# Kernel optimization log

Measured on AMD Instinct MI355X. Metric: run time of the kernel, lower is better.

## Reference

```python
import jax, jax.numpy as jnp
import numpy as np

D_MODEL, D_STATE, D_CONV, D_INNER, DT_RANK, K = 96, 16, 3, 192, 6, 4
B, H, W = 1, 64, 64


def setup_inputs() -> dict:
    key = jax.random.key(0)
    ks = jax.random.split(key, 10)
    x = jax.random.normal(ks[0], (B, H, W, D_MODEL), jnp.float32)
    in_proj_w = jax.random.normal(ks[1], (2 * D_INNER, D_MODEL), jnp.float32) * 0.02
    conv_w = jax.random.normal(ks[2], (D_INNER, 1, D_CONV, D_CONV), jnp.float32) * 0.1
    conv_b = jnp.zeros((D_INNER,), jnp.float32)
    x_proj_w = jax.random.normal(ks[3], (K, DT_RANK + 2 * D_STATE, D_INNER), jnp.float32) * 0.02
    dt_std = DT_RANK ** -0.5
    dt_w = jax.random.uniform(ks[4], (K, D_INNER, DT_RANK), jnp.float32, -dt_std, dt_std)
    # dt bias init: inv-softplus of dt ~ logUniform(1e-3, 1e-1)
    u = jax.random.uniform(ks[5], (K, D_INNER), jnp.float32)
    dt = jnp.exp(u * (np.log(0.1) - np.log(0.001)) + np.log(0.001)).clip(1e-4)
    dt_b = dt + jnp.log(-jnp.expm1(-dt))
    A_logs = jnp.log(jnp.broadcast_to(jnp.arange(1, D_STATE + 1, dtype=jnp.float32), (K * D_INNER, D_STATE)))
    Ds = jnp.ones((K * D_INNER,), jnp.float32)
    ln_g = jnp.ones((D_INNER,), jnp.float32)
    ln_b = jnp.zeros((D_INNER,), jnp.float32)
    out_proj_w = jax.random.normal(ks[6], (D_MODEL, D_INNER), jnp.float32) * 0.02
    return dict(x=x, in_proj_w=in_proj_w, conv_w=conv_w, conv_b=conv_b, x_proj_w=x_proj_w,
                dt_w=dt_w, dt_b=dt_b, A_logs=A_logs, Ds=Ds, ln_g=ln_g, ln_b=ln_b,
                out_proj_w=out_proj_w)


def _ss2d(x, in_proj_w, conv_w, conv_b, x_proj_w, dt_w, dt_b, A_logs, Ds, ln_g, ln_b, out_proj_w):
    b, h, w, c = x.shape
    L = h * w
    d = conv_w.shape[0]            # d_inner
    n = A_logs.shape[1]            # d_state
    r = dt_w.shape[2]              # dt_rank
    # in_proj + split
    xz = jnp.einsum('bhwc,ec->bhwe', x, in_proj_w)
    xx, z = xz[..., :d], xz[..., d:]
    # depthwise conv (NCHW) + SiLU
    xc = xx.transpose(0, 3, 1, 2)
    pad = (D_CONV - 1) // 2
    xc = jax.lax.conv_general_dilated(xc, conv_w, (1, 1), [(pad, pad), (pad, pad)],
                                      feature_group_count=d) + conv_b[None, :, None, None]
    xc = jax.nn.silu(xc)
    # 4 scan directions: HW, WH, and their reverses
    x_hw = xc.reshape(b, d, L)
    x_wh = xc.transpose(0, 1, 3, 2).reshape(b, d, L)
    xs = jnp.stack([x_hw, x_wh, x_hw[..., ::-1], x_wh[..., ::-1]], axis=1)  # (b,K,d,L)
    x_dbl = jnp.einsum('bkdl,kcd->bkcl', xs, x_proj_w)
    dts, Bs, Cs = x_dbl[:, :, :r], x_dbl[:, :, r:r + n], x_dbl[:, :, r + n:]
    dts = jnp.einsum('bkrl,kdr->bkdl', dts, dt_w)
    delta = jax.nn.softplus(dts + dt_b[None, :, :, None])        # (b,K,d,L)
    A = -jnp.exp(A_logs).reshape(K, d, n)
    # time-major scanned inputs
    dA = jnp.exp(jnp.einsum('bkdl,kdn->lbkdn', delta, A))        # (L,b,K,d,n)
    dBu = jnp.einsum('bkdl,bknl,bkdl->lbkdn', delta, Bs, xs)
    Ct = Cs.transpose(3, 0, 1, 2)                                # (L,b,K,n)
    def step(hst, inp):
        dA_t, dBu_t, C_t = inp
        hst = dA_t * hst + dBu_t
        return hst, jnp.einsum('bkdn,bkn->bkd', hst, C_t)
    h0 = jnp.zeros((b, K, d, n), jnp.float32)
    _, ys = jax.lax.scan(step, h0, (dA, dBu, Ct))                # ys: (L,b,K,d)
    out_y = ys.transpose(1, 2, 3, 0) + xs * Ds.reshape(K, d)[None, :, :, None]
    # recombine directions
    inv = out_y[:, 2:4][..., ::-1]
    y1 = out_y[:, 0]
    y2 = inv[:, 0]
    wh = out_y[:, 1].reshape(b, d, w, h).transpose(0, 1, 3, 2).reshape(b, d, L)
    invwh = inv[:, 1].reshape(b, d, w, h).transpose(0, 1, 3, 2).reshape(b, d, L)
    y = (y1 + y2 + wh + invwh).transpose(0, 2, 1).reshape(b, h, w, d)
    # LayerNorm (eps=1e-5, torch default)
    mu = y.mean(-1, keepdims=True)
    var = ((y - mu) ** 2).mean(-1, keepdims=True)
    y = (y - mu) * jax.lax.rsqrt(var + 1e-5) * ln_g + ln_b
    y = y * jax.nn.silu(z)
    return jnp.einsum('bhwd,cd->bhwc', y, out_proj_w)


def reference(x, in_proj_w, conv_w, conv_b, x_proj_w, dt_w, dt_b, A_logs, Ds, ln_g, ln_b, out_proj_w):
    return _ss2d(x, in_proj_w, conv_w, conv_b, x_proj_w, dt_w, dt_b, A_logs, Ds, ln_g, ln_b, out_proj_w)
```

## Files before the change

kernel.cpp:

```cpp
#include <hip/hip_runtime.h>
#include <hip/hip_bf16.h>

#define LL 4096
#define DM 96
#define DI 192
#define NS 16
#define RK 6
#define RKP 8
#define KD 4
#define CPROJ 38
#define NCH (KD*DI)
#define NC (KD*DI*NS)
#define PT 32
#define WS 196
#define OT 8
#define L2E 1.44269504f

__device__ __forceinline__ float bf2f(unsigned short u){
  unsigned int x = ((unsigned int)u) << 16;
  return __uint_as_float(x);
}
__device__ __forceinline__ float b2f(__hip_bfloat16 v){ return __bfloat162float(v); }

__device__ __forceinline__ void detect_bf16(const unsigned short* __restrict__ xh, int tid, int* sflag){
  if (tid < 64){
    unsigned short u = xh[2*tid];
    int e = (u >> 7) & 0xFF;
    int sane = (e >= 107 && e <= 131) ? 1 : 0;
    unsigned long long m = __ballot(sane);
    if (tid == 0) *sflag = (__popcll(m) >= 32) ? 1 : 0;
  }
}

__device__ __forceinline__ int dir_map(int k, int t){
  if (k==0) return t;
  if (k==1) return ((t&63)<<6) | (t>>6);
  if (k==2) return 4095 - t;
  int u = 4095 - t; return ((u&63)<<6) | (u>>6);
}

struct P12 { const void* p[12]; };

__global__ void __launch_bounds__(384) k_inprojcvt(P12 ptrs, float* __restrict__ cvt,
                         float* __restrict__ xx, float* __restrict__ z) {
  __shared__ float xr[8*DM];
  __shared__ int sflag;
  int tid = threadIdx.x;
  detect_bf16((const unsigned short*)ptrs.p[0], tid, &sflag);
  __syncthreads();
  int f = sflag;
  if (blockIdx.x >= LL/8){
    const int off[12] = {0,36864,38592,38784,67968,72576,73344,85632,86400,86592,86784,105216};
    int i = (blockIdx.x - LL/8)*384 + tid + 36864;
    if (i < 105216){
      int j = 1;
      #pragma unroll
      for (int s = 2; s < 11; s++) if (i >= off[s]) j = s;
      int e = i - off[j];
      const void* src = ptrs.p[j+1];
      cvt[i] = f ? b2f(((const __hip_bfloat16*)src)[e]) : ((const float*)src)[e];
    }
    return;
  }
  int l0 = blockIdx.x * 8;
  if (f){
    const __hip_bfloat16* xb = (const __hip_bfloat16*)ptrs.p[0] + (size_t)l0*DM;
    for (int i = tid; i < 8*DM; i += 384) xr[i] = b2f(xb[i]);
  } else {
    const float* xf = (const float*)ptrs.p[0] + (size_t)l0*DM;
    for (int i = tid; i < 8*DM; i += 384) xr[i] = xf[i];
  }
  __syncthreads();
  int e = tid;
  float acc[8];
  #pragma unroll
  for (int i=0;i<8;i++) acc[i]=0.f;
  const float4* xr4 = (const float4*)xr;
  if (f){
    const ushort4* wb = (const ushort4*)((const unsigned short*)ptrs.p[1] + (size_t)e*DM);
    #pragma unroll 4
    for (int c4=0;c4<DM/4;c4++){
      ushort4 uv = wb[c4];
      float4 wv = make_float4(bf2f(uv.x), bf2f(uv.y), bf2f(uv.z), bf2f(uv.w));
      #pragma unroll
      for (int i=0;i<8;i++){
        float4 xv = xr4[i*24 + c4];
        acc[i] = fmaf(wv.x,xv.x,fmaf(wv.y,xv.y,fmaf(wv.z,xv.z,fmaf(wv.w,xv.w,acc[i]))));
      }
    }
  } else {
    const float4* wr4 = (const float4*)((const float*)ptrs.p[1] + (size_t)e*DM);
    #pragma unroll 4
    for (int c4=0;c4<DM/4;c4++){
      float4 wv = wr4[c4];
      #pragma unroll
      for (int i=0;i<8;i++){
        float4 xv = xr4[i*24 + c4];
        acc[i] = fmaf(wv.x,xv.x,fmaf(wv.y,xv.y,fmaf(wv.z,xv.z,fmaf(wv.w,xv.w,acc[i]))));
      }
    }
  }
  if (e < DI) {
    #pragma unroll
    for (int i=0;i<8;i++) xx[(l0+i)*DI + e] = acc[i];
  } else {
    int e2 = e - DI;
    #pragma unroll
    for (int i=0;i<8;i++) z[(l0+i)*DI + e2] = acc[i];
  }
}

__global__ void k_conv(const float* __restrict__ xx,
                       const float* __restrict__ cw,
                       const float* __restrict__ cb,
                       float* __restrict__ xc) {
  int l = blockIdx.x;
  int d = threadIdx.x;
  int h = l >> 6, w = l & 63;
  float acc = cb[d];
  #pragma unroll
  for (int ki=0; ki<3; ki++){
    int hh = h + ki - 1;
    if ((unsigned)hh >= 64u) continue;
    #pragma unroll
    for (int kj=0;kj<3;kj++){
      int wj = w + kj - 1;
      if ((unsigned)wj >= 64u) continue;
      acc = fmaf(cw[d*9 + ki*3 + kj], xx[(hh*64+wj)*DI + d], acc);
    }
  }
  float v = acc / (1.f + __expf(-acc));
  xc[l*DI + d] = v;
}

__global__ void __launch_bounds__(256) k_proj(const float* __restrict__ xc,
                       const float* __restrict__ xpw,
                       float* __restrict__ dts,
                       float* __restrict__ Bb, float* __restrict__ Cb) {
  __shared__ float wl[CPROJ*WS];
  __shared__ float xs[PT*WS];
  int b = blockIdx.x;
  int k = b >> 7;
  int t_base = (b & 127) * PT;
  int tid = threadIdx.x;
  for (int idx = tid; idx < CPROJ*DI; idx += 256){
    int cc = idx / DI, j = idx - cc*DI;
    wl[cc*WS + j] = xpw[(k*CPROJ + cc)*DI + j];
  }
  for (int idx = tid; idx < PT*DI; idx += 256){
    int tt = idx / DI, j = idx - tt*DI;
    xs[tt*WS + j] = xc[dir_map(k, t_base + tt)*DI + j];
  }
  __syncthreads();
  int tg = tid & 7;
  int ty = tid >> 3;
  int cc0 = ty;
  int has2 = (ty + 32 < CPROJ);
  int cc1 = has2 ? (ty + 32) : ty;
  float a0x=0.f,a0y=0.f,a0z=0.f,a0w=0.f;
  float a1x=0.f,a1y=0.f,a1z=0.f,a1w=0.f;
  const float4* w0p = (const float4*)&wl[cc0*WS];
  const float4* w1p = (const float4*)&wl[cc1*WS];
  const float4* x0p = (const float4*)&xs[(tg     )*WS];
  const float4* x1p = (const float4*)&xs[(tg +  8)*WS];
  const float4* x2p = (const float4*)&xs[(tg + 16)*WS];
  const float4* x3p = (const float4*)&xs[(tg + 24)*WS];
  #pragma unroll 4
  for (int jc = 0; jc < DI/4; jc++){
    float4 w0 = w0p[jc], w1 = w1p[jc];
    float4 x0 = x0p[jc], x1 = x1p[jc], x2 = x2p[jc], x3 = x3p[jc];
    a0x = fmaf(w0.x,x0.x,fmaf(w0.y,x0.y,fmaf(w0.z,x0.z,fmaf(w0.w,x0.w,a0x))));
    a0y = fmaf(w0.x,x1.x,fmaf(w0.y,x1.y,fmaf(w0.z,x1.z,fmaf(w0.w,x1.w,a0y))));
    a0z = fmaf(w0.x,x2.x,fmaf(w0.y,x2.y,fmaf(w0.z,x2.z,fmaf(w0.w,x2.w,a0z))));
    a0w = fmaf(w0.x,x3.x,fmaf(w0.y,x3.y,fmaf(w0.z,x3.z,fmaf(w0.w,x3.w,a0w))));
    a1x = fmaf(w1.x,x0.x,fmaf(w1.y,x0.y,fmaf(w1.z,x0.z,fmaf(w1.w,x0.w,a1x))));
    a1y = fmaf(w1.x,x1.x,fmaf(w1.y,x1.y,fmaf(w1.z,x1.z,fmaf(w1.w,x1.w,a1y))));
    a1z = fmaf(w1.x,x2.x,fmaf(w1.y,x2.y,fmaf(w1.z,x2.z,fmaf(w1.w,x2.w,a1z))));
    a1w = fmaf(w1.x,x3.x,fmaf(w1.y,x3.y,fmaf(w1.z,x3.z,fmaf(w1.w,x3.w,a1w))));
  }
  float accs0[4] = {a0x,a0y,a0z,a0w};
  float accs1[4] = {a1x,a1y,a1z,a1w};
  #pragma unroll
  for (int i=0;i<4;i++){
    int t = t_base + tg + 8*i;
    size_t kt = (size_t)k*LL + t;
    {
      int cc = cc0; float v = accs0[i];
      if (cc < RK)            dts[kt*RKP + cc] = v;
      else if (cc < RK+NS)    Bb [kt*NS + (cc-RK)] = v;
      else                    Cb [kt*NS + (cc-RK-NS)] = v;
    }
    if (has2){
      int cc = ty + 32; float v = accs1[i];
      if (cc < RK+NS)         Bb [kt*NS + (cc-RK)] = v;
      else                    Cb [kt*NS + (cc-RK-NS)] = v;
    }
  }
}

template<int CHB>
__global__ void __launch_bounds__(192) k_scanA(
                      const float* __restrict__ xc,
                      const float* __restrict__ dts,
                      const float* __restrict__ Bbuf,
                      const float* __restrict__ A_logs,
                      const float* __restrict__ dtw,
                      const float* __restrict__ dtb,
                      float* __restrict__ cumDbuf,
                      float* __restrict__ Harr) {
  constexpr int CS = LL >> CHB;
  __shared__ float ds_[CS*RKP];
  __shared__ float Bs[CS*NS];
  int b = blockIdx.x;
  int k = b >> CHB;
  int c = b & ((1<<CHB)-1);
  int t0 = c*CS;
  int d = threadIdx.x;
  int kd = k*DI + d;
  for (int i = d; i < CS*RKP; i += 192) ds_[i] = dts[((size_t)k*LL + t0)*RKP + i];
  for (int i = d; i < CS*NS;  i += 192) Bs[i]  = Bbuf[((size_t)k*LL + t0)*NS + i];
  float bt = dtb[kd];
  float w0 = dtw[kd*RK+0], w1 = dtw[kd*RK+1], w2 = dtw[kd*RK+2];
  float w3 = dtw[kd*RK+3], w4 = dtw[kd*RK+4], w5 = dtw[kd*RK+5];
  float A2[16], h[16];
  {
    const float4* ap = (const float4*)&A_logs[kd*NS];
    #pragma unroll
    for (int i=0;i<4;i++){
      float4 av = ap[i];
      A2[4*i+0] = -__expf(av.x)*L2E; A2[4*i+1] = -__expf(av.y)*L2E;
      A2[4*i+2] = -__expf(av.z)*L2E; A2[4*i+3] = -__expf(av.w)*L2E;
    }
  }
  #pragma unroll
  for (int n=0;n<16;n++) h[n] = 0.f;
  __syncthreads();
  float cumD = 0.f;
  #pragma unroll 2
  for (int s=0; s<CS; s++){
    float4 lo = *(const float4*)(ds_ + s*RKP);
    float4 hi = *(const float4*)(ds_ + s*RKP + 4);
    float v = bt;
    v = fmaf(w0, lo.x, v); v = fmaf(w1, lo.y, v); v = fmaf(w2, lo.z, v);
    v = fmaf(w3, lo.w, v); v = fmaf(w4, hi.x, v); v = fmaf(w5, hi.y, v);
    float sp = (v > 20.f) ? v : __logf(1.f + __expf(v));
    cumD += sp;
    int row = dir_map(k, t0 + s);
    float sx = sp * xc[(size_t)row*DI + d];
    float4 b0 = *(const float4*)(Bs + s*NS);
    float4 b1 = *(const float4*)(Bs + s*NS + 4);
    float4 b2 = *(const float4*)(Bs + s*NS + 8);
    float4 b3 = *(const float4*)(Bs + s*NS + 12);
    float bb[16] = {b0.x,b0.y,b0.z,b0.w, b1.x,b1.y,b1.z,b1.w,
                    b2.x,b2.y,b2.z,b2.w, b3.x,b3.y,b3.z,b3.w};
    #pragma unroll
    for (int n=0;n<16;n++){
      float a = exp2f(sp*A2[n]);
      h[n] = fmaf(a, h[n], sx*bb[n]);
    }
  }
  cumDbuf[(size_t)c*NCH + kd] = cumD;
  float4* hp = (float4*)(Harr + ((size_t)c*NCH + kd)*16);
  hp[0] = make_float4(h[0],h[1],h[2],h[3]);
  hp[1] = make_float4(h[4],h[5],h[6],h[7]);
  hp[2] = make_float4(h[8],h[9],h[10],h[11]);
  hp[3] = make_float4(h[12],h[13],h[14],h[15]);
}

template<int CHB>
__global__ void __launch_bounds__(512) k_scan2(const float* __restrict__ A_logs,
                                               const float* __restrict__ cumDbuf,
                                               float* __restrict__ Harr) {
  constexpr int CH = 1 << CHB;
  constexpr int CHP = CH + 1;
  __shared__ float hs[64][CHP];
  __shared__ float cds[4][CH];
  int tid = threadIdx.x;
  int base = blockIdx.x * 64;
  int kd0 = blockIdx.x * 4;
  for (int i4 = tid; i4 < 16*CH; i4 += 512){
    int c = i4 >> 4;
    int jv = (i4 & 15) * 4;
    float4 v = *(const float4*)&Harr[(size_t)c*NC + base + jv];
    hs[jv][c] = v.x; hs[jv+1][c] = v.y; hs[jv+2][c] = v.z; hs[jv+3][c] = v.w;
  }
  for (int i = tid; i < 4*CH; i += 512){
    int c = i >> 2, kdl = i & 3;
    cds[kdl][c] = cumDbuf[(size_t)c*NCH + kd0 + kdl];
  }
  __syncthreads();
  if (tid < 64){
    float A2 = -__expf(A_logs[base + tid]) * L2E;
    const float* cd = cds[tid >> 4];
    float* hr = hs[tid];
    float h = 0.f;
    #pragma unroll 4
    for (int c = 0; c < CH; c++){
      float hl = hr[c];
      float P = exp2f(A2 * cd[c]);
      hr[c] = h;
      h = fmaf(P, h, hl);
    }
  }
  __syncthreads();
  for (int i4 = tid; i4 < 16*CH; i4 += 512){
    int c = i4 >> 4;
    int jv = (i4 & 15) * 4;
    float4 v = make_float4(hs[jv][c], hs[jv+1][c], hs[jv+2][c], hs[jv+3][c]);
    *(float4*)&Harr[(size_t)c*NC + base + jv] = v;
  }
}

template<int CHB>
__global__ void __launch_bounds__(192) k_scanB(
                      const float* __restrict__ xc,
                      const float* __restrict__ dts,
                      const float* __restrict__ Bbuf,
                      const float* __restrict__ Cbuf,
                      const float* __restrict__ A_logs,
                      const float* __restrict__ dtw,
                      const float* __restrict__ dtb,
                      const float* __restrict__ Harr,
                      float* __restrict__ ydir) {
  constexpr int CS = LL >> CHB;
  __shared__ float ds_[CS*RKP];
  __shared__ float Bs[CS*NS];
  __shared__ float Cs[CS*NS];
  int b = blockIdx.x;
  int k = b >> CHB;
  int c = b & ((1<<CHB)-1);
  int t0 = c*CS;
  int d = threadIdx.x;
  int kd = k*DI + d;
  for (int i = d; i < CS*RKP; i += 192) ds_[i] = dts[((size_t)k*LL + t0)*RKP + i];
  for (int i = d; i < CS*NS;  i += 192) Bs[i]  = Bbuf[((size_t)k*LL + t0)*NS + i];
  for (int i = d; i < CS*NS;  i += 192) Cs[i]  = Cbuf[((size_t)k*LL + t0)*NS + i];
  float bt = dtb[kd];
  float w0 = dtw[kd*RK+0], w1 = dtw[kd*RK+1], w2 = dtw[kd*RK+2];
  float w3 = dtw[kd*RK+3], w4 = dtw[kd*RK+4], w5 = dtw[kd*RK+5];
  float A2[16], h[16];
  {
    const float4* ap = (const float4*)&A_logs[kd*NS];
    #pragma unroll
    for (int i=0;i<4;i++){
      float4 av = ap[i];
      A2[4*i+0] = -__expf(av.x)*L2E; A2[4*i+1] = -__expf(av.y)*L2E;
      A2[4*i+2] = -__expf(av.z)*L2E; A2[4*i+3] = -__expf(av.w)*L2E;
    }
  }
  {
    const float4* hp = (const float4*)(Harr + ((size_t)c*NCH + kd)*16);
    float4 h0 = hp[0], h1 = hp[1], h2 = hp[2], h3 = hp[3];
    h[0]=h0.x; h[1]=h0.y; h[2]=h0.z; h[3]=h0.w;
    h[4]=h1.x; h[5]=h1.y; h[6]=h1.z; h[7]=h1.w;
    h[8]=h2.x; h[9]=h2.y; h[10]=h2.z; h[11]=h2.w;
    h[12]=h3.x; h[13]=h3.y; h[14]=h3.z; h[15]=h3.w;
  }
  __syncthreads();
  #pragma unroll 2
  for (int s=0; s<CS; s++){
    float4 lo = *(const float4*)(ds_ + s*RKP);
    float4 hi = *(const float4*)(ds_ + s*RKP + 4);
    float v = bt;
    v = fmaf(w0, lo.x, v); v = fmaf(w1, lo.y, v); v = fmaf(w2, lo.z, v);
    v = fmaf(w3, lo.w, v); v = fmaf(w4, hi.x, v); v = fmaf(w5, hi.y, v);
    float sp = (v > 20.f) ? v : __logf(1.f + __expf(v));
    int row = dir_map(k, t0 + s);
    float sx = sp * xc[(size_t)row*DI + d];
    float4 b0 = *(const float4*)(Bs + s*NS);
    float4 b1 = *(const float4*)(Bs + s*NS + 4);
    float4 b2 = *(const float4*)(Bs + s*NS + 8);
    float4 b3 = *(const float4*)(Bs + s*NS + 12);
    float bb[16] = {b0.x,b0.y,b0.z,b0.w, b1.x,b1.y,b1.z,b1.w,
                    b2.x,b2.y,b2.z,b2.w, b3.x,b3.y,b3.z,b3.w};
    #pragma unroll
    for (int n=0;n<16;n++){
      float a = exp2f(sp*A2[n]);
      h[n] = fmaf(a, h[n], sx*bb[n]);
    }
    float4 c0 = *(const float4*)(Cs + s*NS);
    float4 c1 = *(const float4*)(Cs + s*NS + 4);
    float4 c2 = *(const float4*)(Cs + s*NS + 8);
    float4 c3 = *(const float4*)(Cs + s*NS + 12);
    float cc[16] = {c0.x,c0.y,c0.z,c0.w, c1.x,c1.y,c1.z,c1.w,
                    c2.x,c2.y,c2.z,c2.w, c3.x,c3.y,c3.z,c3.w};
    float y0=0.f, y1=0.f, y2=0.f, y3=0.f;
    #pragma unroll
    for (int n=0;n<4;n++){
      y0 = fmaf(h[4*n+0], cc[4*n+0], y0);
      y1 = fmaf(h[4*n+1], cc[4*n+1], y1);
      y2 = fmaf(h[4*n+2], cc[4*n+2], y2);
      y3 = fmaf(h[4*n+3], cc[4*n+3], y3);
    }
    ydir[((size_t)k*LL + row)*DI + d] = (y0+y1)+(y2+y3);
  }
}

__global__ void __launch_bounds__(192) k_out(
                      const float* __restrict__ ydir,
                      const float* __restrict__ xc,
                      const float* __restrict__ z,
                      const float* __restrict__ Ds,
                      const float* __restrict__ ln_g,
                      const float* __restrict__ ln_b,
                      const float* __restrict__ opw,
                      void* __restrict__ out,
                      const unsigned short* __restrict__ xh) {
  __shared__ float gs[OT*WS];
  __shared__ float ps[2][OT][24];
  __shared__ float mv[2][OT];
  __shared__ int sflag;
  int tid = threadIdx.x;
  int d = tid;
  detect_bf16(xh, tid, &sflag);
  int l0 = blockIdx.x * OT;
  float dsum = Ds[d] + Ds[DI+d] + Ds[2*DI+d] + Ds[3*DI+d];
  #pragma unroll
  for (int r=0;r<OT;r++){
    size_t ld = (size_t)(l0+r)*DI + d;
    float y = ydir[ld]
            + ydir[(size_t)LL*DI   + ld]
            + ydir[(size_t)2*LL*DI + ld]
            + ydir[(size_t)3*LL*DI + ld];
    gs[r*WS + d] = fmaf(xc[ld], dsum, y);
  }
  __syncthreads();
  {
    int r = tid / 24, lane = tid - r*24;
    float s1 = 0.f, s2 = 0.f;
    #pragma unroll
    for (int j = lane; j < DI; j += 24){
      float v = gs[r*WS + j];
      s1 += v; s2 += v*v;
    }
    ps[0][r][lane] = s1; ps[1][r][lane] = s2;
  }
  __syncthreads();
  if (tid < OT){
    float a = 0.f, bb = 0.f;
    #pragma unroll
    for (int j=0;j<24;j++){ a += ps[0][tid][j]; bb += ps[1][tid][j]; }
    float mu = a * (1.f/192.f);
    float var = bb * (1.f/192.f) - mu*mu;
    mv[0][tid] = mu; mv[1][tid] = rsqrtf(var + 1e-5f);
  }
  __syncthreads();
  float lg = ln_g[d], lb = ln_b[d];
  #pragma unroll
  for (int r=0;r<OT;r++){
    float yn = (gs[r*WS + d] - mv[0][r]) * mv[1][r] * lg + lb;
    float zv = z[(size_t)(l0+r)*DI + d];
    gs[r*WS + d] = yn * (zv / (1.f + __expf(-zv)));
  }
  __syncthreads();
  int half = tid / 96;
  int e = tid - half*96;
  int r0 = half*4;
  float acc[4];
  #pragma unroll
  for (int i=0;i<4;i++) acc[i] = 0.f;
  const float4* wrow = (const float4*)(opw + e*DI);
  #pragma unroll 4
  for (int jc = 0; jc < DI/4; jc++){
    float4 w = wrow[jc];
    #pragma unroll
    for (int i=0;i<4;i++){
      float4 gv = *(const float4*)&gs[(r0+i)*WS + jc*4];
      acc[i] = fmaf(w.x,gv.x,fmaf(w.y,gv.y,fmaf(w.z,gv.z,fmaf(w.w,gv.w,acc[i]))));
    }
  }
  int f = sflag;
  #pragma unroll
  for (int i=0;i<4;i++){
    int l = l0 + r0 + i;
    if (f) ((__hip_bfloat16*)out)[l*DM + e] = __float2bfloat16(acc[i]);
    else   ((float*)out)[l*DM + e] = acc[i];
  }
}

extern "C" void kernel_launch(void* const* d_in, const int* in_sizes, int n_in,
                              void* d_out, int out_size, void* d_ws, size_t ws_size,
                              hipStream_t stream) {
  float* ws = (float*)d_ws;
  float* cvt = ws + 16;
  const int off[12] = {0,36864,38592,38784,67968,72576,73344,85632,86400,86592,86784,105216};
  float* c[12];
  c[0] = nullptr;
  for (int i = 1; i < 12; i++) c[i] = cvt + off[i-1];

  float* xx   = cvt + 105216;
  float* z    = xx + (size_t)LL*DI;
  float* xc   = z  + (size_t)LL*DI;
  float* dts  = xc + (size_t)LL*DI;
  float* Bb   = dts + (size_t)KD*LL*RKP;
  float* Cb   = Bb + (size_t)KD*LL*NS;
  float* cumD = Cb + (size_t)KD*LL*NS;

  size_t fixed = 16 + 105216 + 3*(size_t)LL*DI + (size_t)KD*LL*RKP
               + 2*(size_t)KD*LL*NS + (size_t)KD*LL*DI;
  size_t need8 = (fixed + 256*(size_t)(NCH + NC)) * 4;
  int chBits = (ws_size >= need8) ? 8 : 6;
  int CHn = 1 << chBits;
  float* Harr = cumD + (size_t)CHn*NCH;
  float* ydir = Harr + (size_t)CHn*NC;

  P12 ptrs;
  for (int i = 0; i < 12; i++) ptrs.p[i] = d_in[i];

  k_inprojcvt<<<LL/8 + 178, 384, 0, stream>>>(ptrs, cvt, xx, z);
  k_conv<<<LL, DI, 0, stream>>>(xx, c[2], c[3], xc);
  k_proj<<<KD*(LL/PT), 256, 0, stream>>>(xc, c[4], dts, Bb, Cb);
  if (chBits == 8){
    k_scanA<8><<<KD*256, 192, 0, stream>>>(xc, dts, Bb, c[7], c[5], c[6], cumD, Harr);
    k_scan2<8><<<NCH/4, 512, 0, stream>>>(c[7], cumD, Harr);
    k_scanB<8><<<KD*256, 192, 0, stream>>>(xc, dts, Bb, Cb, c[7], c[5], c[6], Harr, ydir);
  } else {
    k_scanA<6><<<KD*64, 192, 0, stream>>>(xc, dts, Bb, c[7], c[5], c[6], cumD, Harr);
    k_scan2<6><<<NCH/4, 512, 0, stream>>>(c[7], cumD, Harr);
    k_scanB<6><<<KD*64, 192, 0, stream>>>(xc, dts, Bb, Cb, c[7], c[5], c[6], Harr, ydir);
  }
  k_out<<<LL/OT, 192, 0, stream>>>(ydir, xc, z, c[8], c[9], c[10], c[11], d_out,
                                   (const unsigned short*)d_in[0]);
}
```

Baseline: 200.0 us.

## Fuse x_proj into chunked scan passes, recomputing projection per pass

Result: no change. 202.2 us (+1.1%).

```diff
diff --git a/kernel.cpp b/kernel.cpp
--- a/kernel.cpp
+++ b/kernel.cpp
@@ -14,6 +14,9 @@
 #define PT 32
 #define WS 196
 #define OT 8
+#define CHB 7
+#define CHN (1<<CHB)
+#define CS (LL>>CHB)
 #define L2E 1.44269504f
 
 __device__ __forceinline__ float bf2f(unsigned short u){
@@ -129,149 +132,171 @@
       acc = fmaf(cw[d*9 + ki*3 + kj], xx[(hh*64+wj)*DI + d], acc);
     }
   }
-  float v = acc / (1.f + __expf(-acc));
-  xc[l*DI + d] = v;
-}
-
-__global__ void __launch_bounds__(256) k_proj(const float* __restrict__ xc,
-                       const float* __restrict__ xpw,
-                       float* __restrict__ dts,
-                       float* __restrict__ Bb, float* __restrict__ Cb) {
-  __shared__ float wl[CPROJ*WS];
-  __shared__ float xs[PT*WS];
-  int b = blockIdx.x;
-  int k = b >> 7;
-  int t_base = (b & 127) * PT;
-  int tid = threadIdx.x;
-  for (int idx = tid; idx < CPROJ*DI; idx += 256){
-    int cc = idx / DI, j = idx - cc*DI;
-    wl[cc*WS + j] = xpw[(k*CPROJ + cc)*DI + j];
-  }
-  for (int idx = tid; idx < PT*DI; idx += 256){
-    int tt = idx / DI, j = idx - tt*DI;
-    xs[tt*WS + j] = xc[dir_map(k, t_base + tt)*DI + j];
-  }
-  __syncthreads();
-  int tg = tid & 7;
-  int ty = tid >> 3;
-  int cc0 = ty;
-  int has2 = (ty + 32 < CPROJ);
-  int cc1 = has2 ? (ty + 32) : ty;
-  float a0x=0.f,a0y=0.f,a0z=0.f,a0w=0.f;
-  float a1x=0.f,a1y=0.f,a1z=0.f,a1w=0.f;
-  const float4* w0p = (const float4*)&wl[cc0*WS];
-  const float4* w1p = (const float4*)&wl[cc1*WS];
-  const float4* x0p = (const float4*)&xs[(tg     )*WS];
-  const float4* x1p = (const float4*)&xs[(tg +  8)*WS];
-  const float4* x2p = (const float4*)&xs[(tg + 16)*WS];
-  const float4* x3p = (const float4*)&xs[(tg + 24)*WS];
-  #pragma unroll 4
-  for (int jc = 0; jc < DI/4; jc++){
-    float4 w0 = w0p[jc], w1 = w1p[jc];
-    float4 x0 = x0p[jc], x1 = x1p[jc], x2 = x2p[jc], x3 = x3p[jc];
-    a0x = fmaf(w0.x,x0.x,fmaf(w0.y,x0.y,fmaf(w0.z,x0.z,fmaf(w0.w,x0.w,a0x))));
-    a0y = fmaf(w0.x,x1.x,fmaf(w0.y,x1.y,fmaf(w0.z,x1.z,fmaf(w0.w,x1.w,a0y))));
-    a0z = fmaf(w0.x,x2.x,fmaf(w0.y,x2.y,fmaf(w0.z,x2.z,fmaf(w0.w,x2.w,a0z))));
-    a0w = fmaf(w0.x,x3.x,fmaf(w0.y,x3.y,fmaf(w0.z,x3.z,fmaf(w0.w,x3.w,a0w))));
-    a1x = fmaf(w1.x,x0.x,fmaf(w1.y,x0.y,fmaf(w1.z,x0.z,fmaf(w1.w,x0.w,a1x))));
-    a1y = fmaf(w1.x,x1.x,fmaf(w1.y,x1.y,fmaf(w1.z,x1.z,fmaf(w1.w,x1.w,a1y))));
-    a1z = fmaf(w1.x,x2.x,fmaf(w1.y,x2.y,fmaf(w1.z,x2.z,fmaf(w1.w,x2.w,a1z))));
-    a1w = fmaf(w1.x,x3.x,fmaf(w1.y,x3.y,fmaf(w1.z,x3.z,fmaf(w1.w,x3.w,a1w))));
-  }
-  float accs0[4] = {a0x,a0y,a0z,a0w};
-  float accs1[4] = {a1x,a1y,a1z,a1w};
-  #pragma unroll
-  for (int i=0;i<4;i++){
-    int t = t_base + tg + 8*i;
-    size_t kt = (size_t)k*LL + t;
-    {
-      int cc = cc0; float v = accs0[i];
-      if (cc < RK)            dts[kt*RKP + cc] = v;
-      else if (cc < RK+NS)    Bb [kt*NS + (cc-RK)] = v;
-      else                    Cb [kt*NS + (cc-RK-NS)] = v;
-    }
-    if (has2){
-      int cc = ty + 32; float v = accs1[i];
-      if (cc < RK+NS)         Bb [kt*NS + (cc-RK)] = v;
-      else                    Cb [kt*NS + (cc-RK-NS)] = v;
-    }
-  }
-}
-
-template<int CHB>
-__global__ void __launch_bounds__(192) k_scanA(
+  xc[l*DI + d] = acc / (1.f + __expf(-acc));
+}
+
+template<int MODE>
+__global__ void __launch_bounds__(256) k_projscan(
                       const float* __restrict__ xc,
-                      const float* __restrict__ dts,
-                      const float* __restrict__ Bbuf,
+                      const float* __restrict__ xpw,
                       const float* __restrict__ A_logs,
                       const float* __restrict__ dtw,
                       const float* __restrict__ dtb,
                       float* __restrict__ cumDbuf,
-                      float* __restrict__ Harr) {
-  constexpr int CS = LL >> CHB;
-  __shared__ float ds_[CS*RKP];
-  __shared__ float Bs[CS*NS];
+                      float* __restrict__ Harr,
+                      float* __restrict__ ydir) {
+  __shared__ float wl[CPROJ*WS];
+  __shared__ float xs[PT*WS];
+  __shared__ float ds_[PT*RKP];
+  __shared__ float Bs[PT*NS];
+  __shared__ float Cs[PT*NS];
   int b = blockIdx.x;
-  int k = b >> CHB;
-  int c = b & ((1<<CHB)-1);
-  int t0 = c*CS;
-  int d = threadIdx.x;
-  int kd = k*DI + d;
-  for (int i = d; i < CS*RKP; i += 192) ds_[i] = dts[((size_t)k*LL + t0)*RKP + i];
-  for (int i = d; i < CS*NS;  i += 192) Bs[i]  = Bbuf[((size_t)k*LL + t0)*NS + i];
-  float bt = dtb[kd];
-  float w0 = dtw[kd*RK+0], w1 = dtw[kd*RK+1], w2 = dtw[kd*RK+2];
-  float w3 = dtw[kd*RK+3], w4 = dtw[kd*RK+4], w5 = dtw[kd*RK+5];
-  float A2[16], h[16];
+  int k = b >> 7;
+  int c = b & 127;
+  int t_base = c * PT;
+  int tid = threadIdx.x;
+
+  for (int idx = tid; idx < CPROJ*DI; idx += 256){
+    int cc = idx / DI, j = idx - cc*DI;
+    wl[cc*WS + j] = xpw[(k*CPROJ + cc)*DI + j];
+  }
+  for (int idx = tid; idx < PT*DI; idx += 256){
+    int tt = idx / DI, j = idx - tt*DI;
+    xs[tt*WS + j] = xc[(size_t)dir_map(k, t_base + tt)*DI + j];
+  }
+  __syncthreads();
+
   {
-    const float4* ap = (const float4*)&A_logs[kd*NS];
+    int tg = tid & 7;
+    int ty = tid >> 3;
+    int cc0 = ty;
+    int has2 = (ty + 32 < CPROJ);
+    int cc1 = has2 ? (ty + 32) : ty;
+    float a0x=0.f,a0y=0.f,a0z=0.f,a0w=0.f;
+    float a1x=0.f,a1y=0.f,a1z=0.f,a1w=0.f;
+    const float4* w0p = (const float4*)&wl[cc0*WS];
+    const float4* w1p = (const float4*)&wl[cc1*WS];
+    const float4* x0p = (const float4*)&xs[(tg     )*WS];
+    const float4* x1p = (const float4*)&xs[(tg +  8)*WS];
+    const float4* x2p = (const float4*)&xs[(tg + 16)*WS];
+    const float4* x3p = (const float4*)&xs[(tg + 24)*WS];
+    #pragma unroll 4
+    for (int jc = 0; jc < DI/4; jc++){
+      float4 w0 = w0p[jc], w1 = w1p[jc];
+      float4 x0 = x0p[jc], x1 = x1p[jc], x2 = x2p[jc], x3 = x3p[jc];
+      a0x = fmaf(w0.x,x0.x,fmaf(w0.y,x0.y,fmaf(w0.z,x0.z,fmaf(w0.w,x0.w,a0x))));
+      a0y = fmaf(w0.x,x1.x,fmaf(w0.y,x1.y,fmaf(w0.z,x1.z,fmaf(w0.w,x1.w,a0y))));
+      a0z = fmaf(w0.x,x2.x,fmaf(w0.y,x2.y,fmaf(w0.z,x2.z,fmaf(w0.w,x2.w,a0z))));
+      a0w = fmaf(w0.x,x3.x,fmaf(w0.y,x3.y,fmaf(w0.z,x3.z,fmaf(w0.w,x3.w,a0w))));
+      a1x = fmaf(w1.x,x0.x,fmaf(w1.y,x0.y,fmaf(w1.z,x0.z,fmaf(w1.w,x0.w,a1x))));
+      a1y = fmaf(w1.x,x1.x,fmaf(w1.y,x1.y,fmaf(w1.z,x1.z,fmaf(w1.w,x1.w,a1y))));
+      a1z = fmaf(w1.x,x2.x,fmaf(w1.y,x2.y,fmaf(w1.z,x2.z,fmaf(w1.w,x2.w,a1z))));
+      a1w = fmaf(w1.x,x3.x,fmaf(w1.y,x3.y,fmaf(w1.z,x3.z,fmaf(w1.w,x3.w,a1w))));
+    }
+    float accs0[4] = {a0x,a0y,a0z,a0w};
+    float accs1[4] = {a1x,a1y,a1z,a1w};
     #pragma unroll
     for (int i=0;i<4;i++){
-      float4 av = ap[i];
-      A2[4*i+0] = -__expf(av.x)*L2E; A2[4*i+1] = -__expf(av.y)*L2E;
-      A2[4*i+2] = -__expf(av.z)*L2E; A2[4*i+3] = -__expf(av.w)*L2E;
-    }
-  }
-  #pragma unroll
-  for (int n=0;n<16;n++) h[n] = 0.f;
-  __syncthreads();
-  float cumD = 0.f;
-  #pragma unroll 2
-  for (int s=0; s<CS; s++){
-    float4 lo = *(const float4*)(ds_ + s*RKP);
-    float4 hi = *(const float4*)(ds_ + s*RKP + 4);
-    float v = bt;
-    v = fmaf(w0, lo.x, v); v = fmaf(w1, lo.y, v); v = fmaf(w2, lo.z, v);
-    v = fmaf(w3, lo.w, v); v = fmaf(w4, hi.x, v); v = fmaf(w5, hi.y, v);
-    float sp = (v > 20.f) ? v : __logf(1.f + __expf(v));
-    cumD += sp;
-    int row = dir_map(k, t0 + s);
-    float sx = sp * xc[(size_t)row*DI + d];
-    float4 b0 = *(const float4*)(Bs + s*NS);
-    float4 b1 = *(const float4*)(Bs + s*NS + 4);
-    float4 b2 = *(const float4*)(Bs + s*NS + 8);
-    float4 b3 = *(const float4*)(Bs + s*NS + 12);
-    float bb[16] = {b0.x,b0.y,b0.z,b0.w, b1.x,b1.y,b1.z,b1.w,
-                    b2.x,b2.y,b2.z,b2.w, b3.x,b3.y,b3.z,b3.w};
-    #pragma unroll
-    for (int n=0;n<16;n++){
-      float a = exp2f(sp*A2[n]);
-      h[n] = fmaf(a, h[n], sx*bb[n]);
-    }
-  }
-  cumDbuf[(size_t)c*NCH + kd] = cumD;
-  float4* hp = (float4*)(Harr + ((size_t)c*NCH + kd)*16);
-  hp[0] = make_float4(h[0],h[1],h[2],h[3]);
-  hp[1] = make_float4(h[4],h[5],h[6],h[7]);
-  hp[2] = make_float4(h[8],h[9],h[10],h[11]);
-  hp[3] = make_float4(h[12],h[13],h[14],h[15]);
-}
-
-template<int CHB>
+      int t = tg + 8*i;
+      {
+        int cc = cc0; float v = accs0[i];
+        if (cc < RK)            ds_[t*RKP + cc] = v;
+        else if (cc < RK+NS)    Bs [t*NS + (cc-RK)] = v;
+        else                    Cs [t*NS + (cc-RK-NS)] = v;
+      }
+      if (has2){
+        int cc = ty + 32; float v = accs1[i];
+        if (cc < RK+NS)         Bs [t*NS + (cc-RK)] = v;
+        else                    Cs [t*NS + (cc-RK-NS)] = v;
+      }
+    }
+  }
+  __syncthreads();
+
+  if (tid < DI){
+    int d = tid;
+    int kd = k*DI + d;
+    float bt = dtb[kd];
+    float w0 = dtw[kd*RK+0], w1 = dtw[kd*RK+1], w2 = dtw[kd*RK+2];
+    float w3 = dtw[kd*RK+3], w4 = dtw[kd*RK+4], w5 = dtw[kd*RK+5];
+    float A2[16], h[16];
+    {
+      const float4* ap = (const float4*)&A_logs[kd*NS];
+      #pragma unroll
+      for (int i=0;i<4;i++){
+        float4 av = ap[i];
+        A2[4*i+0] = -__expf(av.x)*L2E; A2[4*i+1] = -__expf(av.y)*L2E;
+        A2[4*i+2] = -__expf(av.z)*L2E; A2[4*i+3] = -__expf(av.w)*L2E;
+      }
+    }
+    if (MODE == 0){
+      #pragma unroll
+      for (int n=0;n<16;n++) h[n] = 0.f;
+    } else {
+      const float4* hp = (const float4*)(Harr + ((size_t)c*NCH + kd)*16);
+      float4 h0 = hp[0], h1 = hp[1], h2 = hp[2], h3 = hp[3];
+      h[0]=h0.x; h[1]=h0.y; h[2]=h0.z; h[3]=h0.w;
+      h[4]=h1.x; h[5]=h1.y; h[6]=h1.z; h[7]=h1.w;
+      h[8]=h2.x; h[9]=h2.y; h[10]=h2.z; h[11]=h2.w;
+      h[12]=h3.x; h[13]=h3.y; h[14]=h3.z; h[15]=h3.w;
+    }
+    float cumD = 0.f;
+    #pragma unroll 2
+    for (int s=0; s<CS; s++){
+      float4 lo = *(const float4*)(ds_ + s*RKP);
+      float4 hi = *(const float4*)(ds_ + s*RKP + 4);
+      float v = bt;
+      v = fmaf(w0, lo.x, v); v = fmaf(w1, lo.y, v); v = fmaf(w2, lo.z, v);
+      v = fmaf(w3, lo.w, v); v = fmaf(w4, hi.x, v); v = fmaf(w5, hi.y, v);
+      float sp = (v > 20.f) ? v : __logf(1.f + __expf(v));
+      if (MODE == 0) cumD += sp;
+      float sx = sp * xs[s*WS + d];
+      float4 b0 = *(const float4*)(Bs + s*NS);
+      float4 b1 = *(const float4*)(Bs + s*NS + 4);
+      float4 b2 = *(const float4*)(Bs + s*NS + 8);
+      float4 b3 = *(const float4*)(Bs + s*NS + 12);
+      float bb[16] = {b0.x,b0.y,b0.z,b0.w, b1.x,b1.y,b1.z,b1.w,
+                      b2.x,b2.y,b2.z,b2.w, b3.x,b3.y,b3.z,b3.w};
+      #pragma unroll
+      for (int n=0;n<16;n++){
+        float aa = exp2f(sp*A2[n]);
+        h[n] = fmaf(aa, h[n], sx*bb[n]);
+      }
+      if (MODE == 1){
+        float4 c0 = *(const float4*)(Cs + s*NS);
+        float4 c1 = *(const float4*)(Cs + s*NS + 4);
+        float4 c2 = *(const float4*)(Cs + s*NS + 8);
+        float4 c3 = *(const float4*)(Cs + s*NS + 12);
+        float cc[16] = {c0.x,c0.y,c0.z,c0.w, c1.x,c1.y,c1.z,c1.w,
+                        c2.x,c2.y,c2.z,c2.w, c3.x,c3.y,c3.z,c3.w};
+        float y0=0.f, y1=0.f, y2=0.f, y3=0.f;
+        #pragma unroll
+        for (int n=0;n<4;n++){
+          y0 = fmaf(h[4*n+0], cc[4*n+0], y0);
+          y1 = fmaf(h[4*n+1], cc[4*n+1], y1);
+          y2 = fmaf(h[4*n+2], cc[4*n+2], y2);
+          y3 = fmaf(h[4*n+3], cc[4*n+3], y3);
+        }
+        int row = dir_map(k, t_base + s);
+        ydir[((size_t)k*LL + row)*DI + d] = (y0+y1)+(y2+y3);
+      }
+    }
+    if (MODE == 0){
+      cumDbuf[(size_t)c*NCH + kd] = cumD;
+      float4* hp = (float4*)(Harr + ((size_t)c*NCH + kd)*16);
+      hp[0] = make_float4(h[0],h[1],h[2],h[3]);
+      hp[1] = make_float4(h[4],h[5],h[6],h[7]);
+      hp[2] = make_float4(h[8],h[9],h[10],h[11]);
+      hp[3] = make_float4(h[12],h[13],h[14],h[15]);
+    }
+  }
+}
+
+template<int CB>
 __global__ void __launch_bounds__(512) k_scan2(const float* __restrict__ A_logs,
                                                const float* __restrict__ cumDbuf,
                                                float* __restrict__ Harr) {
-  constexpr int CH = 1 << CHB;
+  constexpr int CH = 1 << CB;
   constexpr int CHP = CH + 1;
   __shared__ float hs[64][CHP];
   __shared__ float cds[4][CH];
@@ -308,91 +333,6 @@
     int jv = (i4 & 15) * 4;
     float4 v = make_float4(hs[jv][c], hs[jv+1][c], hs[jv+2][c], hs[jv+3][c]);
     *(float4*)&Harr[(size_t)c*NC + base + jv] = v;
-  }
-}
-
-template<int CHB>
-__global__ void __launch_bounds__(192) k_scanB(
-                      const float* __restrict__ xc,
-                      const float* __restrict__ dts,
-                      const float* __restrict__ Bbuf,
-                      const float* __restrict__ Cbuf,
-                      const float* __restrict__ A_logs,
-                      const float* __restrict__ dtw,
-                      const float* __restrict__ dtb,
-                      const float* __restrict__ Harr,
-                      float* __restrict__ ydir) {
-  constexpr int CS = LL >> CHB;
-  __shared__ float ds_[CS*RKP];
-  __shared__ float Bs[CS*NS];
-  __shared__ float Cs[CS*NS];
-  int b = blockIdx.x;
-  int k = b >> CHB;
-  int c = b & ((1<<CHB)-1);
-  int t0 = c*CS;
-  int d = threadIdx.x;
-  int kd = k*DI + d;
-  for (int i = d; i < CS*RKP; i += 192) ds_[i] = dts[((size_t)k*LL + t0)*RKP + i];
-  for (int i = d; i < CS*NS;  i += 192) Bs[i]  = Bbuf[((size_t)k*LL + t0)*NS + i];
-  for (int i = d; i < CS*NS;  i += 192) Cs[i]  = Cbuf[((size_t)k*LL + t0)*NS + i];
-  float bt = dtb[kd];
-  float w0 = dtw[kd*RK+0], w1 = dtw[kd*RK+1], w2 = dtw[kd*RK+2];
-  float w3 = dtw[kd*RK+3], w4 = dtw[kd*RK+4], w5 = dtw[kd*RK+5];
-  float A2[16], h[16];
-  {
-    const float4* ap = (const float4*)&A_logs[kd*NS];
-    #pragma unroll
-    for (int i=0;i<4;i++){
-      float4 av = ap[i];
-      A2[4*i+0] = -__expf(av.x)*L2E; A2[4*i+1] = -__expf(av.y)*L2E;
-      A2[4*i+2] = -__expf(av.z)*L2E; A2[4*i+3] = -__expf(av.w)*L2E;
-    }
-  }
-  {
-    const float4* hp = (const float4*)(Harr + ((size_t)c*NCH + kd)*16);
-    float4 h0 = hp[0], h1 = hp[1], h2 = hp[2], h3 = hp[3];
-    h[0]=h0.x; h[1]=h0.y; h[2]=h0.z; h[3]=h0.w;
-    h[4]=h1.x; h[5]=h1.y; h[6]=h1.z; h[7]=h1.w;
-    h[8]=h2.x; h[9]=h2.y; h[10]=h2.z; h[11]=h2.w;
-    h[12]=h3.x; h[13]=h3.y; h[14]=h3.z; h[15]=h3.w;
-  }
-  __syncthreads();
-  #pragma unroll 2
-  for (int s=0; s<CS; s++){
-    float4 lo = *(const float4*)(ds_ + s*RKP);
-    float4 hi = *(const float4*)(ds_ + s*RKP + 4);
-    float v = bt;
-    v = fmaf(w0, lo.x, v); v = fmaf(w1, lo.y, v); v = fmaf(w2, lo.z, v);
-    v = fmaf(w3, lo.w, v); v = fmaf(w4, hi.x, v); v = fmaf(w5, hi.y, v);
-    float sp = (v > 20.f) ? v : __logf(1.f + __expf(v));
-    int row = dir_map(k, t0 + s);
-    float sx = sp * xc[(size_t)row*DI + d];
-    float4 b0 = *(const float4*)(Bs + s*NS);
-    float4 b1 = *(const float4*)(Bs + s*NS + 4);
-    float4 b2 = *(const float4*)(Bs + s*NS + 8);
-    float4 b3 = *(const float4*)(Bs + s*NS + 12);
-    float bb[16] = {b0.x,b0.y,b0.z,b0.w, b1.x,b1.y,b1.z,b1.w,
-                    b2.x,b2.y,b2.z,b2.w, b3.x,b3.y,b3.z,b3.w};
-    #pragma unroll
-    for (int n=0;n<16;n++){
-      float a = exp2f(sp*A2[n]);
-      h[n] = fmaf(a, h[n], sx*bb[n]);
-    }
-    float4 c0 = *(const float4*)(Cs + s*NS);
-    float4 c1 = *(const float4*)(Cs + s*NS + 4);
-    float4 c2 = *(const float4*)(Cs + s*NS + 8);
-    float4 c3 = *(const float4*)(Cs + s*NS + 12);
-    float cc[16] = {c0.x,c0.y,c0.z,c0.w, c1.x,c1.y,c1.z,c1.w,
-                    c2.x,c2.y,c2.z,c2.w, c3.x,c3.y,c3.z,c3.w};
-    float y0=0.f, y1=0.f, y2=0.f, y3=0.f;
-    #pragma unroll
-    for (int n=0;n<4;n++){
-      y0 = fmaf(h[4*n+0], cc[4*n+0], y0);
-      y1 = fmaf(h[4*n+1], cc[4*n+1], y1);
-      y2 = fmaf(h[4*n+2], cc[4*n+2], y2);
-      y3 = fmaf(h[4*n+3], cc[4*n+3], y3);
-    }
-    ydir[((size_t)k*LL + row)*DI + d] = (y0+y1)+(y2+y3);
   }
 }
 
@@ -491,34 +431,20 @@
   float* xx   = cvt + 105216;
   float* z    = xx + (size_t)LL*DI;
   float* xc   = z  + (size_t)LL*DI;
-  float* dts  = xc + (size_t)LL*DI;
-  float* Bb   = dts + (size_t)KD*LL*RKP;
-  float* Cb   = Bb + (size_t)KD*LL*NS;
-  float* cumD = Cb + (size_t)KD*LL*NS;
-
-  size_t fixed = 16 + 105216 + 3*(size_t)LL*DI + (size_t)KD*LL*RKP
-               + 2*(size_t)KD*LL*NS + (size_t)KD*LL*DI;
-  size_t need8 = (fixed + 256*(size_t)(NCH + NC)) * 4;
-  int chBits = (ws_size >= need8) ? 8 : 6;
-  int CHn = 1 << chBits;
-  float* Harr = cumD + (size_t)CHn*NCH;
-  float* ydir = Harr + (size_t)CHn*NC;
+  float* cumD = xc + (size_t)LL*DI;
+  float* Harr = cumD + (size_t)CHN*NCH;
+  float* ydir = Harr + (size_t)CHN*NC;
 
   P12 ptrs;
   for (int i = 0; i < 12; i++) ptrs.p[i] = d_in[i];
 
   k_inprojcvt<<<LL/8 + 178, 384, 0, stream>>>(ptrs, cvt, xx, z);
   k_conv<<<LL, DI, 0, stream>>>(xx, c[2], c[3], xc);
-  k_proj<<<KD*(LL/PT), 256, 0, stream>>>(xc, c[4], dts, Bb, Cb);
-  if (chBits == 8){
-    k_scanA<8><<<KD*256, 192, 0, stream>>>(xc, dts, Bb, c[7], c[5], c[6], cumD, Harr);
-    k_scan2<8><<<NCH/4, 512, 0, stream>>>(c[7], cumD, Harr);
-    k_scanB<8><<<KD*256, 192, 0, stream>>>(xc, dts, Bb, Cb, c[7], c[5], c[6], Harr, ydir);
-  } else {
-    k_scanA<6><<<KD*64, 192, 0, stream>>>(xc, dts, Bb, c[7], c[5], c[6], cumD, Harr);
-    k_scan2<6><<<NCH/4, 512, 0, stream>>>(c[7], cumD, Harr);
-    k_scanB<6><<<KD*64, 192, 0, stream>>>(xc, dts, Bb, Cb, c[7], c[5], c[6], Harr, ydir);
-  }
+  k_projscan<0><<<KD*CHN, 256, 0, stream>>>(xc, c[4], c[7], c[5], c[6],
+                                            cumD, Harr, nullptr);
+  k_scan2<CHB><<<NCH/4, 512, 0, stream>>>(c[7], cumD, Harr);
+  k_projscan<1><<<KD*CHN, 256, 0, stream>>>(xc, c[4], c[7], c[5], c[6],
+                                            cumD, Harr, ydir);
   k_out<<<LL/OT, 192, 0, stream>>>(ydir, xc, z, c[8], c[9], c[10], c[11], d_out,
                                    (const unsigned short*)d_in[0]);
 }
```
